# Kernel optimization log

Hardware: AMD Instinct MI355X
Metric: run time of the kernel (lower is better)

The kernel has to match this reference:

```python
import jax, jax.numpy as jnp
import numpy as np

N_NODES = 50000
N_EDGES = 800000
IN_C, HID_C, OUT_C = 256, 256, 128


def setup_inputs() -> dict:
    key = jax.random.key(0)
    k1, k2, k3, k4 = jax.random.split(key, 4)
    x = jax.random.normal(k1, (N_NODES, IN_C), dtype=jnp.float32)
    edge_index = jax.random.randint(k2, (2, N_EDGES), 0, N_NODES, dtype=jnp.int64)
    # Glorot-ish init for linear weights, zero bias (PyG GCNConv default)
    W1 = jax.random.normal(k3, (IN_C, HID_C), dtype=jnp.float32) / np.sqrt(IN_C)
    b1 = jnp.zeros((HID_C,), dtype=jnp.float32)
    W2 = jax.random.normal(k4, (HID_C, OUT_C), dtype=jnp.float32) / np.sqrt(HID_C)
    b2 = jnp.zeros((OUT_C,), dtype=jnp.float32)
    return {"x": x, "edge_index": edge_index, "W1": W1, "b1": b1, "W2": W2, "b2": b2}


def _gcn_conv(x, src, dst, norm, W, b):
    # Linear transform first (dense GEMM), then normalized scatter-add aggregation.
    h = x @ W                                   # [N, out]
    msg = h[src] * norm[:, None]                # [E+N, out] gathered, scaled messages
    out = jax.ops.segment_sum(msg, dst, num_segments=x.shape[0])
    return out + b


def reference(x, edge_index, W1, b1, W2, b2):
    n = x.shape[0]
    loops = jnp.arange(n, dtype=edge_index.dtype)
    # PyG GCNConv: add self-loops, symmetric normalization D^-1/2 A D^-1/2
    src = jnp.concatenate([edge_index[0], loops])
    dst = jnp.concatenate([edge_index[1], loops])
    deg = jnp.zeros((n,), dtype=x.dtype).at[dst].add(1.0)
    dinv = jnp.where(deg > 0, jax.lax.rsqrt(deg), 0.0)
    norm = dinv[src] * dinv[dst]                # [E+N]
    h = jax.nn.relu(_gcn_conv(x, src, dst, norm, W1, b1))
    return _gcn_conv(h, src, dst, norm, W2, b2)
```

## Files before the change

kernel.cpp:

```cpp
#include <hip/hip_runtime.h>


#define NN 50000
#define EE 800000
#define IN_C 256
#define HID_C 256
#define OUT_C 128
#define CAP 64

typedef __attribute__((ext_vector_type(8))) short short8;
typedef __attribute__((ext_vector_type(4))) float f32x4;

static __device__ __forceinline__ ushort f2b(float f) {
    union { float f; unsigned u; } v; v.f = f;
    unsigned r = v.u + 0x7FFF + ((v.u >> 16) & 1);
    return (ushort)(r >> 16);
}
static __device__ __forceinline__ float b2f(ushort u) {
    union { float f; unsigned u; } v; v.u = ((unsigned)u) << 16;
    return v.f;
}


__global__ void fill_kernel(const int* __restrict__ src, const int* __restrict__ dst,
                            int* __restrict__ cnt, int* __restrict__ slots, int e) {
    int i = blockIdx.x * blockDim.x + threadIdx.x;
    if (i < e) {
        int s = src[i], d = dst[i];
        int pos = atomicAdd(&cnt[d], 1);
        if (pos < CAP) slots[(size_t)d * CAP + pos] = s;
    }
}


__global__ void cvt_kernel(const float4* __restrict__ in, ushort4* __restrict__ out, int n4) {
    int i = blockIdx.x * blockDim.x + threadIdx.x;
    if (i < n4) {
        float4 v = in[i];
        ushort4 o;
        o.x = f2b(v.x); o.y = f2b(v.y); o.z = f2b(v.z); o.w = f2b(v.w);
        out[i] = o;
    }
}

__global__ void zero_sent_kernel(ushort* __restrict__ hb, ushort* __restrict__ h2b) {
    int t = threadIdx.x;
    ushort4 z = {0, 0, 0, 0};
    if (t < 64) ((ushort4*)(hb + (size_t)NN * HID_C))[t] = z;
    else if (t < 96) ((ushort4*)(h2b + (size_t)NN * OUT_C))[t - 64] = z;
}

__global__ __launch_bounds__(256) void gemm_bf16_kernel(
    const ushort* __restrict__ A, const float* __restrict__ W,
    const int* __restrict__ cnt, ushort* __restrict__ C, int M, int Ntot) {
    constexpr int KK = 256;
    __shared__ ushort wt[128 * KK];

    const int tid = threadIdx.x;
    const int rowBase = blockIdx.x * 128;
    const int colBase = blockIdx.y * 128;

    for (int it = 0; it < 32; ++it) {
        int item = tid + it * 256;
        int n = item & 127;
        int kg = item >> 7;
        int k = kg * 4;
        const float* wp = W + (size_t)k * Ntot + colBase + n;
        ushort4 o;
        o.x = f2b(wp[0]);
        o.y = f2b(wp[Ntot]);
        o.z = f2b(wp[2 * Ntot]);
        o.w = f2b(wp[3 * Ntot]);
        *(ushort4*)((char*)wt + n * 512 + ((kg * 8) ^ ((n & 7) << 4))) = o;
    }
    __syncthreads();

    const int wave = tid >> 6, lane = tid & 63;
    const int l15 = lane & 15, lk = lane >> 4;

    int r0 = rowBase + wave * 32 + l15;
    int ra0 = min(r0, M - 1);
    int ra1 = min(r0 + 16, M - 1);
    const ushort* Ar0 = A + (size_t)ra0 * KK + lk * 8;
    const ushort* Ar1 = A + (size_t)ra1 * KK + lk * 8;

    f32x4 acc[2][8] = {};

#pragma unroll
    for (int ks = 0; ks < KK / 32; ++ks) {
        short8 a0 = *(const short8*)(Ar0 + ks * 32);
        short8 a1 = *(const short8*)(Ar1 + ks * 32);
        int kbyte = ks * 64 + lk * 16;
#pragma unroll
        for (int nt = 0; nt < 8; ++nt) {
            int n = nt * 16 + l15;
            short8 b = *(const short8*)((const char*)wt + n * 512 + (kbyte ^ ((n & 7) << 4)));
            acc[0][nt] = __builtin_amdgcn_mfma_f32_16x16x32_bf16(a0, b, acc[0][nt], 0, 0, 0);
            acc[1][nt] = __builtin_amdgcn_mfma_f32_16x16x32_bf16(a1, b, acc[1][nt], 0, 0, 0);
        }
    }

#pragma unroll
    for (int t = 0; t < 2; ++t) {
        int rbase = rowBase + wave * 32 + t * 16 + lk * 4;
#pragma unroll
        for (int r = 0; r < 4; ++r) {
            int row = rbase + r;
            if (row < M) {
                float dv = rsqrtf((float)(cnt[row] + 1));
#pragma unroll
                for (int nt = 0; nt < 8; ++nt)
                    C[(size_t)row * Ntot + colBase + nt * 16 + l15] = f2b(acc[t][nt][r] * dv);
            }
        }
    }
}


template <int C, bool RELU, bool OUT_BF16>
__global__ __launch_bounds__(256) void gather_kernel(
    const ushort* __restrict__ h, const int* __restrict__ cnt,
    const int* __restrict__ slots, const float* __restrict__ bias,
    void* __restrict__ out, int n) {
    constexpr int VPL = C / 64;
    const int node = blockIdx.x * 4 + (threadIdx.x >> 6);
    if (node >= n) return;
    const int lane = threadIdx.x & 63;
    const int c0 = cnt[node];
    const int deg = min(c0, CAP);
    const int* sl = slots + (size_t)node * CAP;
    const ushort* hl = h + lane * VPL;

    float acc[VPL] = {};
    for (int base = 0; base < deg; base += 16) {
        int4 sa = *(const int4*)(sl + base);
        int4 sb = *(const int4*)(sl + base + 4);
        int4 sc = *(const int4*)(sl + base + 8);
        int4 sd = *(const int4*)(sl + base + 12);
        int id[16];
        id[0] = sa.x; id[1] = sa.y; id[2] = sa.z; id[3] = sa.w;
        id[4] = sb.x; id[5] = sb.y; id[6] = sb.z; id[7] = sb.w;
        id[8] = sc.x; id[9] = sc.y; id[10] = sc.z; id[11] = sc.w;
        id[12] = sd.x; id[13] = sd.y; id[14] = sd.z; id[15] = sd.w;
        int ix[16];
#pragma unroll
        for (int j = 0; j < 16; ++j) ix[j] = (base + j < deg) ? id[j] : n;
        if constexpr (VPL == 4) {
            ushort4 v[16];
#pragma unroll
            for (int j = 0; j < 16; ++j) v[j] = *(const ushort4*)(hl + (size_t)ix[j] * C);
#pragma unroll
            for (int j = 0; j < 16; ++j) {
                acc[0] += b2f(v[j].x); acc[1] += b2f(v[j].y);
                acc[2] += b2f(v[j].z); acc[3] += b2f(v[j].w);
            }
        } else {
            ushort2 v[16];
#pragma unroll
            for (int j = 0; j < 16; ++j) v[j] = *(const ushort2*)(hl + (size_t)ix[j] * C);
#pragma unroll
            for (int j = 0; j < 16; ++j) {
                acc[0] += b2f(v[j].x); acc[1] += b2f(v[j].y);
            }
        }
    }

    if constexpr (VPL == 4) {
        ushort4 v = *(const ushort4*)(hl + (size_t)node * C);
        acc[0] += b2f(v.x); acc[1] += b2f(v.y); acc[2] += b2f(v.z); acc[3] += b2f(v.w);
    } else {
        ushort2 v = *(const ushort2*)(hl + (size_t)node * C);
        acc[0] += b2f(v.x); acc[1] += b2f(v.y);
    }

    const float dv = rsqrtf((float)(c0 + 1));
    const float* bp = bias + lane * VPL;
    float r[VPL];
#pragma unroll
    for (int k = 0; k < VPL; ++k) {
        r[k] = acc[k] * dv + bp[k];
        if (RELU) r[k] = fmaxf(r[k], 0.0f);
    }
    if constexpr (OUT_BF16) {
        ushort* op = (ushort*)out + (size_t)node * C + lane * VPL;
#pragma unroll
        for (int k = 0; k < VPL; ++k) op[k] = f2b(r[k]);
    } else {
        float* op = (float*)out + (size_t)node * C + lane * VPL;
#pragma unroll
        for (int k = 0; k < VPL; ++k) op[k] = r[k];
    }
}


extern "C" void kernel_launch(void* const* d_in, const int* in_sizes, int n_in,
                              void* d_out, int out_size, void* d_ws, size_t ws_size,
                              hipStream_t stream) {
    const float* x  = (const float*)d_in[0];
    const int*   ei = (const int*)d_in[1];
    const float* W1 = (const float*)d_in[2];
    const float* b1 = (const float*)d_in[3];
    const float* W2 = (const float*)d_in[4];
    const float* b2 = (const float*)d_in[5];
    float* out = (float*)d_out;

    const int N = in_sizes[0] / IN_C;
    const int E = in_sizes[1] / 2;
    const int* src = ei;
    const int* dst = ei + E;

    char* ws = (char*)d_ws;
    int*    cnt   = (int*)(ws + (256 << 10));
    int*    slots = (int*)(ws + (512 << 10));
    ushort* xb    = (ushort*)(ws + (size_t)(14 << 20));
    ushort* hb    = (ushort*)(ws + (size_t)(40 << 20));
    ushort* h1b   = (ushort*)(ws + (size_t)(66 << 20));
    ushort* h2b   = (ushort*)(ws + (size_t)(92 << 20));

    hipMemsetAsync(cnt, 0, (size_t)N * sizeof(int), stream);
    fill_kernel<<<(E + 255) / 256, 256, 0, stream>>>(src, dst, cnt, slots, E);

    {
        int n4 = N * IN_C / 4;
        cvt_kernel<<<(n4 + 255) / 256, 256, 0, stream>>>((const float4*)x, (ushort4*)xb, n4);
    }
    zero_sent_kernel<<<1, 128, 0, stream>>>(hb, h2b);

    {
        dim3 grid((N + 127) / 128, HID_C / 128);
        gemm_bf16_kernel<<<grid, 256, 0, stream>>>(xb, W1, cnt, hb, N, HID_C);
    }
    gather_kernel<HID_C, true, true><<<(N + 3) / 4, 256, 0, stream>>>(
        hb, cnt, slots, b1, h1b, N);

    {
        dim3 grid((N + 127) / 128, OUT_C / 128);
        gemm_bf16_kernel<<<grid, 256, 0, stream>>>(h1b, W2, cnt, h2b, N, OUT_C);
    }
    gather_kernel<OUT_C, false, false><<<(N + 3) / 4, 256, 0, stream>>>(
        h2b, cnt, slots, b2, out, N);
}
```

Baseline: 201.7 us.

## Fuse edge-slot fill, input conversion and sentinel zeroing into one XCD-partitioned kernel

Merges the slot-filling, fp32-to-bf16 conversion and sentinel-zeroing kernels into a single launch whose block ranges do different jobs. The fill part assigns each destination-node range to blocks sharing blockIdx&7, assuming round-robin XCD placement, so atomics and slot writes for a node stay within one XCD's L2. Each fill block scans the full dst array and filters, so dst is read eight times. It saves two launches and lets conversion overlap the atomic-heavy fill.

```diff
diff --git a/kernel.cpp b/kernel.cpp
--- a/kernel.cpp
+++ b/kernel.cpp
@@ -7,6 +7,8 @@
 #define HID_C 256
 #define OUT_C 128
 #define CAP 64
+#define FILLB 2048
+#define CVTB 1024
 
 typedef __attribute__((ext_vector_type(8))) short short8;
 typedef __attribute__((ext_vector_type(4))) float f32x4;
@@ -22,32 +24,38 @@
 }
 
 
-__global__ void fill_kernel(const int* __restrict__ src, const int* __restrict__ dst,
-                            int* __restrict__ cnt, int* __restrict__ slots, int e) {
-    int i = blockIdx.x * blockDim.x + threadIdx.x;
-    if (i < e) {
-        int s = src[i], d = dst[i];
-        int pos = atomicAdd(&cnt[d], 1);
-        if (pos < CAP) slots[(size_t)d * CAP + pos] = s;
-    }
-}
-
-
-__global__ void cvt_kernel(const float4* __restrict__ in, ushort4* __restrict__ out, int n4) {
-    int i = blockIdx.x * blockDim.x + threadIdx.x;
-    if (i < n4) {
-        float4 v = in[i];
-        ushort4 o;
-        o.x = f2b(v.x); o.y = f2b(v.y); o.z = f2b(v.z); o.w = f2b(v.w);
-        out[i] = o;
-    }
-}
-
-__global__ void zero_sent_kernel(ushort* __restrict__ hb, ushort* __restrict__ h2b) {
-    int t = threadIdx.x;
-    ushort4 z = {0, 0, 0, 0};
-    if (t < 64) ((ushort4*)(hb + (size_t)NN * HID_C))[t] = z;
-    else if (t < 96) ((ushort4*)(h2b + (size_t)NN * OUT_C))[t - 64] = z;
+__global__ __launch_bounds__(256) void build_kernel(
+    const int* __restrict__ src, const int* __restrict__ dst,
+    int* __restrict__ cnt, int* __restrict__ slots,
+    const float4* __restrict__ x, ushort4* __restrict__ xb,
+    ushort* __restrict__ hb, ushort* __restrict__ h2b, int e, int n4) {
+    const int bid = blockIdx.x;
+    const int tid = threadIdx.x;
+    if (bid < FILLB) {
+        const int xcd = bid & 7;
+        const int lo = xcd * (NN / 8);
+        const int hi = lo + (NN / 8);
+        const int sub = bid >> 3;
+        for (int i = sub * 256 + tid; i < e; i += 256 * 256) {
+            int d = dst[i];
+            if (d >= lo && d < hi) {
+                int s = src[i];
+                int pos = atomicAdd(&cnt[d], 1);
+                if (pos < CAP) slots[(size_t)d * CAP + pos] = s;
+            }
+        }
+    } else if (bid < FILLB + CVTB) {
+        for (int i = (bid - FILLB) * 256 + tid; i < n4; i += CVTB * 256) {
+            float4 v = x[i];
+            ushort4 o;
+            o.x = f2b(v.x); o.y = f2b(v.y); o.z = f2b(v.z); o.w = f2b(v.w);
+            xb[i] = o;
+        }
+    } else {
+        ushort4 z = {0, 0, 0, 0};
+        if (tid < 64) ((ushort4*)(hb + (size_t)NN * HID_C))[tid] = z;
+        else if (tid < 96) ((ushort4*)(h2b + (size_t)NN * OUT_C))[tid - 64] = z;
+    }
 }
 
 __global__ __launch_bounds__(256) void gemm_bf16_kernel(
@@ -218,13 +226,11 @@
     ushort* h2b   = (ushort*)(ws + (size_t)(92 << 20));
 
     hipMemsetAsync(cnt, 0, (size_t)N * sizeof(int), stream);
-    fill_kernel<<<(E + 255) / 256, 256, 0, stream>>>(src, dst, cnt, slots, E);
-
     {
         int n4 = N * IN_C / 4;
-        cvt_kernel<<<(n4 + 255) / 256, 256, 0, stream>>>((const float4*)x, (ushort4*)xb, n4);
-    }
-    zero_sent_kernel<<<1, 128, 0, stream>>>(hb, h2b);
+        build_kernel<<<FILLB + CVTB + 1, 256, 0, stream>>>(
+            src, dst, cnt, slots, (const float4*)x, (ushort4*)xb, hb, h2b, E, n4);
+    }
 
     {
         dim3 grid((N + 127) / 128, HID_C / 128);
```

Result: faster. 193.0 us (-4.3%).
